# Performance work log

Hardware: AMD Instinct MI355X
Metric: run time of the kernel (lower is better)

## Reference

```python
import jax, jax.numpy as jnp
import numpy as np

B, L, D, S = 32, 512, 512, 8  # batch, seq_len, input_dim, slic


def setup_inputs() -> dict:
    key = jax.random.key(0)
    k1, k2, k3, k4, k5, k6 = jax.random.split(key, 6)
    def glorot(k, shape):
        fan_in, fan_out = shape[-2] if len(shape) > 1 else shape[0], shape[-1]
        lim = np.sqrt(6.0 / (fan_in + fan_out)).astype(np.float32)
        return jax.random.uniform(k, shape, jnp.float32, -lim, lim)
    return {
        "arg1": jax.random.normal(k1, (B, L, D), jnp.float32),
        "arg2": jax.random.normal(k2, (B, L, D), jnp.float32),
        "Wg": glorot(k3, (2 * D, S)),
        "Bg": jnp.zeros((S,), jnp.float32),
        "Mr": glorot(k4, (S, D, D)),
        "V": glorot(k5, (2 * D, S)),
        "b": jnp.zeros((S,), jnp.float32),
        "U": glorot(k6, (S,)),
    }


def reference(arg1, arg2, Wg, Bg, Mr, V, b, U):
    d = arg1.shape[-1]
    # concat([w1, w2]) @ W  ==  w1 @ W[:D] + w2 @ W[D:], broadcast over pairs
    g = jax.nn.sigmoid(
        jnp.einsum('bid,ds->bis', arg1, Wg[:d])[:, :, None, :]
        + jnp.einsum('bjd,ds->bjs', arg2, Wg[d:])[:, None, :, :]
        + Bg
    )  # [B, L, L, S]
    # mul3d: for each slice k, w1 @ Mr[k] @ w2^T -> stacked over k
    bi = jnp.einsum('bid,kde,bje->bijk', arg1, Mr, arg2)  # [B, L, L, S]
    si = jax.nn.sigmoid(
        jnp.einsum('bid,ds->bis', arg1, V[:d])[:, :, None, :]
        + jnp.einsum('bjd,ds->bjs', arg2, V[d:])[:, None, :, :]
    )  # [B, L, L, S]
    score = bi * g + si * (1.0 - g) + b  # [B, L, L, S]
    return jax.nn.sigmoid(jnp.einsum('bijk,k->bij', score, U))  # [B, L, L]
```

## Files before the change

### kernel.cpp

```cpp
#include <hip/hip_runtime.h>
#include <math.h>

#define B_ 32
#define L_ 512
#define D_ 512
#define S_ 8

using f16x8 = __attribute__((ext_vector_type(8))) _Float16;
using f32x4 = __attribute__((ext_vector_type(4))) float;

__device__ __forceinline__ float sigm(float x) { return 1.0f / (1.0f + __expf(-x)); }

__device__ __forceinline__ void stage16(const _Float16* g, _Float16* l) {
    __builtin_amdgcn_global_load_lds(
        (const __attribute__((address_space(1))) void*)g,
        (__attribute__((address_space(3))) void*)l, 16, 0, 0);
}

__global__ __launch_bounds__(256) void conv_tiled_kernel(
    const float* __restrict__ in, _Float16* __restrict__ outh)
{
    __shared__ __align__(16) float scr[4096];
    const int t = threadIdx.x;
    const size_t base_in  = (size_t)blockIdx.x * 128 * D_;
    const size_t base_out = (size_t)blockIdx.x * 65536;
    for (int kt = 0; kt < 16; ++kt) {
        if (kt) __syncthreads();
        #pragma unroll
        for (int f = 0; f < 4; ++f) {
            const int fi = t + f * 256;
            const int row = fi >> 3, c4 = fi & 7;
            float4 v = *(const float4*)(in + base_in + (size_t)row * D_ + kt * 32 + c4 * 4);
            *(float4*)(scr + ((c4 >> 1) * 128 + row) * 8 + (c4 & 1) * 4) = v;
        }
        __syncthreads();
        #pragma unroll
        for (int c = 0; c < 2; ++c) {
            const int s = t + c * 256;
            const float4 v0 = *(const float4*)(scr + s * 8);
            const float4 v1 = *(const float4*)(scr + s * 8 + 4);
            const float vv[8] = {v0.x, v0.y, v0.z, v0.w, v1.x, v1.y, v1.z, v1.w};
            f16x8 h;
            #pragma unroll
            for (int i = 0; i < 8; ++i) h[i] = (_Float16)vv[i];
            *(f16x8*)(outh + base_out + kt * 4096 + s * 8) = h;
        }
    }
}

__global__ __launch_bounds__(256) void conv_mrT_kernel(
    const float* __restrict__ Mr, _Float16* __restrict__ out)
{
    __shared__ float tile[32][33];
    const int k = blockIdx.z;
    const int e0 = blockIdx.x * 32, d0 = blockIdx.y * 32;
    const int tx = threadIdx.x & 31, ty = threadIdx.x >> 5;
    #pragma unroll
    for (int i = 0; i < 4; ++i) {
        const int dl = ty + i * 8;
        tile[dl][tx] = Mr[(size_t)k * (D_ * D_) + (size_t)(d0 + dl) * D_ + e0 + tx];
    }
    __syncthreads();
    if (threadIdx.x < 128) {
        const int el = threadIdx.x & 31, dc = threadIdx.x >> 5;
        f16x8 h;
        #pragma unroll
        for (int i = 0; i < 8; ++i) h[i] = (_Float16)tile[dc * 8 + i][el];
        const int e = e0 + el, d = d0 + dc * 8;
        const size_t addr = (size_t)(k * 4 + (e >> 7)) * 65536
                          + (size_t)(d >> 5) * 4096 + ((d >> 3) & 3) * 1024
                          + (size_t)(e & 127) * 8;
        *(f16x8*)(out + addr) = h;
    }
}

__global__ __launch_bounds__(256) void proj_kernel(
    const float* __restrict__ a1, const float* __restrict__ a2,
    const float* __restrict__ Wg, const float* __restrict__ V,
    const float* __restrict__ Bg,
    float* __restrict__ G1, float* __restrict__ G2,
    float* __restrict__ S1, float* __restrict__ S2)
{
    const int wave = threadIdx.x >> 6;
    const int lane = threadIdx.x & 63;
    const int r = blockIdx.x * 4 + wave;
    const float* a1r = a1 + (size_t)r * D_;
    const float* a2r = a2 + (size_t)r * D_;
    float g1[S_] = {}, g2[S_] = {}, s1[S_] = {}, s2[S_] = {};
    for (int d = lane; d < D_; d += 64) {
        float x1 = a1r[d], x2 = a2r[d];
        const float* wga = Wg + d * S_;
        const float* wgb = Wg + (D_ + d) * S_;
        const float* va  = V  + d * S_;
        const float* vb  = V  + (D_ + d) * S_;
        #pragma unroll
        for (int s = 0; s < S_; ++s) {
            g1[s] += x1 * wga[s];
            g2[s] += x2 * wgb[s];
            s1[s] += x1 * va[s];
            s2[s] += x2 * vb[s];
        }
    }
    #pragma unroll
    for (int off = 32; off > 0; off >>= 1) {
        #pragma unroll
        for (int s = 0; s < S_; ++s) {
            g1[s] += __shfl_down(g1[s], off);
            g2[s] += __shfl_down(g2[s], off);
            s1[s] += __shfl_down(s1[s], off);
            s2[s] += __shfl_down(s2[s], off);
        }
    }
    if (lane == 0) {
        #pragma unroll
        for (int s = 0; s < S_; ++s) {
            G1[(size_t)r * S_ + s] = g1[s] + Bg[s];
            G2[(size_t)r * S_ + s] = g2[s];
            S1[(size_t)r * S_ + s] = s1[s];
            S2[(size_t)r * S_ + s] = s2[s];
        }
    }
}

__global__ __launch_bounds__(256) void gemm_a_kernel(
    const _Float16* __restrict__ Ah, const _Float16* __restrict__ Bt,
    _Float16* __restrict__ C, int ytile0, int nY)
{
    __shared__ __align__(16) _Float16 lds[32768];

    const int t = threadIdx.x;
    const int lane = t & 63, wv = t >> 6;
    const int wm = wv >> 1, wn = wv & 1;
    const int q = lane >> 4, i15 = lane & 15;

    int nt, yl;
    {
        const int id = blockIdx.x;
        if (nY >= 8) { const int y0 = id & 7; const int r = id >> 3; nt = r & 31; yl = (r >> 5) * 8 + y0; }
        else         { nt = id & 31; yl = id >> 5; }
    }
    const size_t abase = (size_t)(ytile0 + yl) * 65536;
    const size_t bbase = (size_t)nt * 65536;
    const int kblk = nt >> 2;
    const int e0 = (nt & 3) * 128;
    const int r0 = yl * 128;

    f32x4 acc[4][4];
    const f32x4 zero = {0.f, 0.f, 0.f, 0.f};
    #pragma unroll
    for (int a = 0; a < 4; ++a)
        #pragma unroll
        for (int b = 0; b < 4; ++b) acc[a][b] = zero;

    auto stage_it = [&](int kt2, int buf) {
        _Float16* As = lds + buf * 16384;
        _Float16* Bs = As + 8192;
        const size_t ab = abase + kt2 * 8192;
        const size_t bb = bbase + kt2 * 8192;
        #pragma unroll
        for (int c = 0; c < 4; ++c) {
            const int s8 = t + c * 256;
            stage16(Ah + ab + s8 * 8, As + s8 * 8);
            stage16(Bt + bb + s8 * 8, Bs + s8 * 8);
        }
    };

    stage_it(0, 0);
    __syncthreads();
    for (int kt2 = 0; kt2 < 8; ++kt2) {
        const int cur = kt2 & 1;
        if (kt2 < 7) stage_it(kt2 + 1, cur ^ 1);
        const _Float16* As = lds + cur * 16384;
        const _Float16* Bs = As + 8192;
        #pragma unroll
        for (int kk2 = 0; kk2 < 2; ++kk2) {
            const int kq = kk2 * 4 + q;
            f16x8 bfr[4];
            #pragma unroll
            for (int nn = 0; nn < 4; ++nn)
                bfr[nn] = *(const f16x8*)(Bs + ((size_t)kq * 128 + wn * 64 + nn * 16 + i15) * 8);
            #pragma unroll
            for (int mt = 0; mt < 4; ++mt) {
                const int m = wm * 64 + mt * 16 + i15;
                f16x8 a = *(const f16x8*)(As + ((size_t)kq * 128 + m) * 8);
                #pragma unroll
                for (int nn = 0; nn < 4; ++nn)
                    acc[mt][nn] = __builtin_amdgcn_mfma_f32_16x16x32_f16(a, bfr[nn], acc[mt][nn], 0, 0, 0);
            }
        }
        __syncthreads();
    }

    float* scr = (float*)lds + wv * 1104;
    #pragma unroll
    for (int mt = 0; mt < 4; ++mt) {
        #pragma unroll
        for (int nn = 0; nn < 4; ++nn)
            #pragma unroll
            for (int r = 0; r < 4; ++r)
                scr[(q * 4 + r) * 68 + nn * 16 + i15] = acc[mt][nn][r];
        __builtin_amdgcn_s_waitcnt(0);
        #pragma unroll
        for (int cc = 0; cc < 2; ++cc) {
            const int row = lane & 15;
            const int ech = (lane >> 4) + cc * 4;
            const float4 v0 = *(const float4*)(scr + row * 68 + ech * 8);
            const float4 v1 = *(const float4*)(scr + row * 68 + ech * 8 + 4);
            const float vv[8] = {v0.x, v0.y, v0.z, v0.w, v1.x, v1.y, v1.z, v1.w};
            f16x8 h;
            #pragma unroll
            for (int i = 0; i < 8; ++i) h[i] = (_Float16)vv[i];
            const int e = e0 + wn * 64 + ech * 8;
            const int ig = r0 + wm * 64 + mt * 16 + row;
            const size_t addr = (size_t)(ig >> 4) * 65536
                              + (size_t)(e >> 5) * 4096 + ((e >> 3) & 3) * 1024
                              + (size_t)(kblk * 16 + row) * 8;
            *(f16x8*)(C + addr) = h;
        }
        __builtin_amdgcn_s_waitcnt(0);
    }
}

__global__ __launch_bounds__(256) void gemm_b_kernel(
    const _Float16* __restrict__ A1, const _Float16* __restrict__ a2t,
    const float* __restrict__ G1, const float* __restrict__ G2,
    const float* __restrict__ S1, const float* __restrict__ S2,
    const float* __restrict__ U, const float* __restrict__ bvec,
    float* __restrict__ out, int b0, int NB)
{
    __shared__ __align__(16) _Float16 lds[32768];

    const int t = threadIdx.x;
    const int lane = t & 63, wv = t >> 6;
    const int wm = wv >> 1, wn = wv & 1;
    const int q = lane >> 4, i15 = lane & 15;

    int bl, jt, y;
    {
        const int id = blockIdx.x;
        bl = id & (NB - 1);
        const int r = id / NB;
        jt = r & 3;
        y = r >> 2;
    }
    const int bg = b0 + bl;
    const int j0 = jt * 128;
    const size_t abase = (size_t)(bl * 32 + y) * 65536;
    const size_t bbase = (size_t)(bg * 4 + jt) * 65536;

    f32x4 acc[4][4];
    const f32x4 zero = {0.f, 0.f, 0.f, 0.f};
    #pragma unroll
    for (int a = 0; a < 4; ++a)
        #pragma unroll
        for (int b = 0; b < 4; ++b) acc[a][b] = zero;

    auto stage_it = [&](int kt2, int buf) {
        _Float16* As = lds + buf * 16384;
        _Float16* Bs = As + 8192;
        const size_t ab = abase + kt2 * 8192;
        const size_t bb = bbase + kt2 * 8192;
        #pragma unroll
        for (int c = 0; c < 4; ++c) {
            const int s8 = t + c * 256;
            stage16(A1 + ab + s8 * 8, As + s8 * 8);
            stage16(a2t + bb + s8 * 8, Bs + s8 * 8);
        }
    };

    stage_it(0, 0);
    __syncthreads();
    for (int kt2 = 0; kt2 < 8; ++kt2) {
        const int cur = kt2 & 1;
        if (kt2 < 7) stage_it(kt2 + 1, cur ^ 1);
        const _Float16* As = lds + cur * 16384;
        const _Float16* Bs = As + 8192;
        #pragma unroll
        for (int kk2 = 0; kk2 < 2; ++kk2) {
            const int kq = kk2 * 4 + q;
            f16x8 bfr[4];
            #pragma unroll
            for (int nn = 0; nn < 4; ++nn)
                bfr[nn] = *(const f16x8*)(Bs + ((size_t)kq * 128 + wn * 64 + nn * 16 + i15) * 8);
            #pragma unroll
            for (int mt = 0; mt < 4; ++mt) {
                const int m = wm * 64 + mt * 16 + i15;
                f16x8 a = *(const f16x8*)(As + ((size_t)kq * 128 + m) * 8);
                #pragma unroll
                for (int nn = 0; nn < 4; ++nn)
                    acc[mt][nn] = __builtin_amdgcn_mfma_f32_16x16x32_f16(a, bfr[nn], acc[mt][nn], 0, 0, 0);
            }
        }
        __syncthreads();
    }

    float U4[4];
    float cbias = 0.f;
    #pragma unroll
    for (int k = 0; k < 8; ++k) cbias += U[k] * bvec[k];
    #pragma unroll
    for (int mt = 0; mt < 4; ++mt) U4[mt] = U[wm * 4 + mt];

    float g1v[4][4], s1v[4][4];
    #pragma unroll
    for (int r = 0; r < 4; ++r) {
        const int ig = y * 16 + q * 4 + r;
        const float4 g1 = *(const float4*)(G1 + ((size_t)bg * L_ + ig) * S_ + wm * 4);
        const float4 s1 = *(const float4*)(S1 + ((size_t)bg * L_ + ig) * S_ + wm * 4);
        g1v[r][0] = g1.x; g1v[r][1] = g1.y; g1v[r][2] = g1.z; g1v[r][3] = g1.w;
        s1v[r][0] = s1.x; s1v[r][1] = s1.y; s1v[r][2] = s1.z; s1v[r][3] = s1.w;
    }

    float part[4][4];
    #pragma unroll
    for (int nn = 0; nn < 4; ++nn) {
        const int j = j0 + wn * 64 + nn * 16 + i15;
        const float4 g2 = *(const float4*)(G2 + ((size_t)bg * L_ + j) * S_ + wm * 4);
        const float4 s2 = *(const float4*)(S2 + ((size_t)bg * L_ + j) * S_ + wm * 4);
        const float g2p[4] = {g2.x, g2.y, g2.z, g2.w};
        const float s2p[4] = {s2.x, s2.y, s2.z, s2.w};
        #pragma unroll
        for (int r = 0; r < 4; ++r) {
            float p = 0.f;
            #pragma unroll
            for (int mt = 0; mt < 4; ++mt) {
                const float g  = sigm(g1v[r][mt] + g2p[mt]);
                const float si = sigm(s1v[r][mt] + s2p[mt]);
                p += U4[mt] * (acc[mt][nn][r] * g + si * (1.f - g));
            }
            part[nn][r] = p;
        }
    }

    float* xb = (float*)lds;
    #pragma unroll
    for (int nn = 0; nn < 4; ++nn)
        *(float4*)(xb + t * 16 + nn * 4) = *(const float4*)&part[nn][0];
    __syncthreads();
    if (wm == 0) {
        #pragma unroll
        for (int nn = 0; nn < 4; ++nn) {
            const int j = j0 + wn * 64 + nn * 16 + i15;
            const float4 o = *(const float4*)(xb + (t + 128) * 16 + nn * 4);
            const float op[4] = {o.x, o.y, o.z, o.w};
            #pragma unroll
            for (int r = 0; r < 4; ++r) {
                const int ig = y * 16 + q * 4 + r;
                out[((size_t)bg * L_ + ig) * L_ + j] = sigm(part[nn][r] + op[r] + cbias);
            }
        }
    }
}

extern "C" void kernel_launch(void* const* d_in, const int* in_sizes, int n_in,
                              void* d_out, int out_size, void* d_ws, size_t ws_size,
                              hipStream_t stream)
{
    const float* arg1 = (const float*)d_in[0];
    const float* arg2 = (const float*)d_in[1];
    const float* Wg   = (const float*)d_in[2];
    const float* Bg   = (const float*)d_in[3];
    const float* Mr   = (const float*)d_in[4];
    const float* V    = (const float*)d_in[5];
    const float* bvec = (const float*)d_in[6];
    const float* U    = (const float*)d_in[7];
    float* out = (float*)d_out;

    char* w = (char*)d_ws;
    size_t off = 0;
    auto nxt = [&](size_t bytes) -> void* {
        void* p = w + off;
        off = (off + bytes + 255) & ~(size_t)255;
        return p;
    };

    _Float16* mrT = (_Float16*)nxt((size_t)S_ * D_ * D_ * 2);
    float* G1 = (float*)nxt((size_t)B_ * L_ * S_ * 4);
    float* G2 = (float*)nxt((size_t)B_ * L_ * S_ * 4);
    float* S1 = (float*)nxt((size_t)B_ * L_ * S_ * 4);
    float* S2 = (float*)nxt((size_t)B_ * L_ * S_ * 4);
    _Float16* a1h = (_Float16*)nxt((size_t)B_ * L_ * D_ * 2);
    _Float16* a2h = (_Float16*)nxt((size_t)B_ * L_ * D_ * 2);
    const size_t fixed = off;

    const size_t perA1 = (size_t)L_ * S_ * D_ * 2;
    int NB = 8;
    while (NB > 1 && fixed + (size_t)NB * perA1 + 4096 > ws_size) NB >>= 1;
    _Float16* A1 = (_Float16*)nxt((size_t)NB * perA1);

    conv_mrT_kernel<<<dim3(16, 16, 8), 256, 0, stream>>>(Mr, mrT);
    proj_kernel<<<dim3(B_ * L_ / 4), 256, 0, stream>>>(arg1, arg2, Wg, V, Bg, G1, G2, S1, S2);
    conv_tiled_kernel<<<dim3(B_ * L_ / 128), 256, 0, stream>>>(arg1, a1h);
    conv_tiled_kernel<<<dim3(B_ * L_ / 128), 256, 0, stream>>>(arg2, a2h);

    for (int b0 = 0; b0 < B_; b0 += NB) {
        gemm_a_kernel<<<dim3(32 * NB * 4), 256, 0, stream>>>(a1h, mrT, A1, b0 * 4, NB * 4);
        gemm_b_kernel<<<dim3(NB * 128), 256, 0, stream>>>(
            A1, a2h, G1, G2, S1, S2, U, bvec, out, b0, NB);
    }
}
```

Measured before the change: 497.6 us.

## Compute gate projections with fp16 MFMA and split input conversion across more blocks

Measured after the change: 435.4 us. 12.5% less time.

```diff
diff --git a/kernel.cpp b/kernel.cpp
--- a/kernel.cpp
+++ b/kernel.cpp
@@ -22,10 +22,12 @@
 {
     __shared__ __align__(16) float scr[4096];
     const int t = threadIdx.x;
-    const size_t base_in  = (size_t)blockIdx.x * 128 * D_;
-    const size_t base_out = (size_t)blockIdx.x * 65536;
-    for (int kt = 0; kt < 16; ++kt) {
-        if (kt) __syncthreads();
+    const int rt = blockIdx.x & 127;
+    const int kt0 = (blockIdx.x >> 7) * 4;
+    const size_t base_in  = (size_t)rt * 128 * D_;
+    const size_t base_out = (size_t)rt * 65536;
+    for (int kt = kt0; kt < kt0 + 4; ++kt) {
+        if (kt != kt0) __syncthreads();
         #pragma unroll
         for (int f = 0; f < 4; ++f) {
             const int fi = t + f * 256;
@@ -74,52 +76,54 @@
     }
 }
 
-__global__ __launch_bounds__(256) void proj_kernel(
-    const float* __restrict__ a1, const float* __restrict__ a2,
+__global__ __launch_bounds__(256) void convW_kernel(
     const float* __restrict__ Wg, const float* __restrict__ V,
-    const float* __restrict__ Bg,
+    _Float16* __restrict__ Wt)
+{
+    const int idx = blockIdx.x * 256 + threadIdx.x;
+    const int j = idx & 7;
+    const int n = (idx >> 3) & 15;
+    const int q = (idx >> 7) & 3;
+    const int kt = (idx >> 9) & 15;
+    const int side = idx >> 13;
+    const int d = side * 512 + kt * 32 + q * 8 + j;
+    const float v = (n < 8) ? Wg[d * S_ + n] : V[d * S_ + (n - 8)];
+    Wt[idx] = (_Float16)v;
+}
+
+__global__ __launch_bounds__(256) void proj_mfma_kernel(
+    const _Float16* __restrict__ a1h, const _Float16* __restrict__ a2h,
+    const _Float16* __restrict__ Wt, const float* __restrict__ Bg,
     float* __restrict__ G1, float* __restrict__ G2,
     float* __restrict__ S1, float* __restrict__ S2)
 {
-    const int wave = threadIdx.x >> 6;
-    const int lane = threadIdx.x & 63;
-    const int r = blockIdx.x * 4 + wave;
-    const float* a1r = a1 + (size_t)r * D_;
-    const float* a2r = a2 + (size_t)r * D_;
-    float g1[S_] = {}, g2[S_] = {}, s1[S_] = {}, s2[S_] = {};
-    for (int d = lane; d < D_; d += 64) {
-        float x1 = a1r[d], x2 = a2r[d];
-        const float* wga = Wg + d * S_;
-        const float* wgb = Wg + (D_ + d) * S_;
-        const float* va  = V  + d * S_;
-        const float* vb  = V  + (D_ + d) * S_;
-        #pragma unroll
-        for (int s = 0; s < S_; ++s) {
-            g1[s] += x1 * wga[s];
-            g2[s] += x2 * wgb[s];
-            s1[s] += x1 * va[s];
-            s2[s] += x2 * vb[s];
-        }
-    }
-    #pragma unroll
-    for (int off = 32; off > 0; off >>= 1) {
-        #pragma unroll
-        for (int s = 0; s < S_; ++s) {
-            g1[s] += __shfl_down(g1[s], off);
-            g2[s] += __shfl_down(g2[s], off);
-            s1[s] += __shfl_down(s1[s], off);
-            s2[s] += __shfl_down(s2[s], off);
-        }
-    }
-    if (lane == 0) {
-        #pragma unroll
-        for (int s = 0; s < S_; ++s) {
-            G1[(size_t)r * S_ + s] = g1[s] + Bg[s];
-            G2[(size_t)r * S_ + s] = g2[s];
-            S1[(size_t)r * S_ + s] = s1[s];
-            S2[(size_t)r * S_ + s] = s2[s];
-        }
-    }
+    const int t = threadIdx.x;
+    const int lane = t & 63, wv = t >> 6;
+    const int q = lane >> 4, i15 = lane & 15;
+    const int id = blockIdx.x;
+    const int side = id >> 8;
+    const int rb = id & 255;
+    const int rtile = rb >> 1;
+    const int rbase = (rb & 1) * 64 + wv * 16;
+
+    const _Float16* A = (side ? a2h : a1h) + (size_t)rtile * 65536;
+    const _Float16* W = Wt + side * 8192;
+
+    f32x4 acc = {0.f, 0.f, 0.f, 0.f};
+    #pragma unroll
+    for (int kt = 0; kt < 16; ++kt) {
+        f16x8 a = *(const f16x8*)(A + (size_t)kt * 4096 + q * 1024 + (rbase + i15) * 8);
+        f16x8 b = *(const f16x8*)(W + (size_t)(kt * 4 + q) * 128 + i15 * 8);
+        acc = __builtin_amdgcn_mfma_f32_16x16x32_f16(a, b, acc, 0, 0, 0);
+    }
+
+    float* dst = (i15 < 8) ? (side ? G2 : G1) : (side ? S2 : S1);
+    const int n = i15 & 7;
+    const float add = (side == 0 && i15 < 8) ? Bg[n] : 0.f;
+    const int R0 = rtile * 128 + rbase + q * 4;
+    #pragma unroll
+    for (int r = 0; r < 4; ++r)
+        dst[(size_t)(R0 + r) * S_ + n] = acc[r] + add;
 }
 
 __global__ __launch_bounds__(256) void gemm_a_kernel(
@@ -375,6 +379,7 @@
     };
 
     _Float16* mrT = (_Float16*)nxt((size_t)S_ * D_ * D_ * 2);
+    _Float16* Wt  = (_Float16*)nxt((size_t)2 * 16 * 4 * 16 * 8 * 2);
     float* G1 = (float*)nxt((size_t)B_ * L_ * S_ * 4);
     float* G2 = (float*)nxt((size_t)B_ * L_ * S_ * 4);
     float* S1 = (float*)nxt((size_t)B_ * L_ * S_ * 4);
@@ -389,9 +394,10 @@
     _Float16* A1 = (_Float16*)nxt((size_t)NB * perA1);
 
     conv_mrT_kernel<<<dim3(16, 16, 8), 256, 0, stream>>>(Mr, mrT);
-    proj_kernel<<<dim3(B_ * L_ / 4), 256, 0, stream>>>(arg1, arg2, Wg, V, Bg, G1, G2, S1, S2);
-    conv_tiled_kernel<<<dim3(B_ * L_ / 128), 256, 0, stream>>>(arg1, a1h);
-    conv_tiled_kernel<<<dim3(B_ * L_ / 128), 256, 0, stream>>>(arg2, a2h);
+    conv_tiled_kernel<<<dim3(512), 256, 0, stream>>>(arg1, a1h);
+    conv_tiled_kernel<<<dim3(512), 256, 0, stream>>>(arg2, a2h);
+    convW_kernel<<<dim3(64), 256, 0, stream>>>(Wg, V, Wt);
+    proj_mfma_kernel<<<dim3(512), 256, 0, stream>>>(a1h, a2h, Wt, Bg, G1, G2, S1, S2);
 
     for (int b0 = 0; b0 < B_; b0 += NB) {
         gemm_a_kernel<<<dim3(32 * NB * 4), 256, 0, stream>>>(a1h, mrT, A1, b0 * 4, NB * 4);
```
